# Performance work log

Measured on AMD Instinct MI355X. Metric: run time of the kernel, lower is better.

## Reference

```python
import jax, jax.numpy as jnp
import numpy as np

NUM_HEADS = 16
NEG = -10000000.0


def setup_inputs() -> dict:
    key = jax.random.key(0)
    k1, k2, k3 = jax.random.split(key, 3)
    B, N, C = 4, 2048, 1024
    inputs = jax.random.normal(k1, (B, N, C), dtype=jnp.float32)
    # learned params (xavier-ish scale)
    W_qkv = jax.random.normal(k2, (C, 3 * C), dtype=jnp.float32) * 0.02
    W_proj = jax.random.normal(k3, (C, C), dtype=jnp.float32) * 0.02
    b_proj = jnp.zeros((C,), dtype=jnp.float32)
    attn_mask = jnp.ones((N, N), dtype=jnp.int32)      # >0 means keep
    padding_mask = jnp.zeros((B, N), dtype=jnp.int32)  # >0 means mask out
    return {"inputs": inputs, "attn_mask": attn_mask, "padding_mask": padding_mask,
            "W_qkv": W_qkv, "W_proj": W_proj, "b_proj": b_proj}


def reference(inputs, attn_mask, padding_mask, W_qkv, W_proj, b_proj):
    B, N, C = inputs.shape
    H = NUM_HEADS
    d = C // H
    scale = d ** -0.5
    qkv = inputs @ W_qkv                                   # [B,N,3C]
    qkv = qkv.reshape(B, N, 3, H, d).transpose(2, 0, 3, 1, 4)  # [3,B,H,N,d]
    q, k, v = qkv[0], qkv[1], qkv[2]
    scores = jnp.einsum('bhqd,bhkd->bhqk', q, k) * scale   # [B,H,N,N]
    scores = jnp.where(attn_mask > 0, scores, NEG)
    pm = padding_mask[:, None, None, :]                    # [B,1,1,N]
    scores = jnp.where(pm > 0, NEG, scores)
    attn = jax.nn.softmax(scores, axis=-1)
    x = jnp.einsum('bhqk,bhkd->bhqd', attn, v)             # [B,H,N,d]
    x = x.swapaxes(1, 2).reshape(B, N, C)
    return x @ W_proj + b_proj
```

## Files before the change

kernel.cpp:

```cpp
#include <hip/hip_runtime.h>

#define NEG -10000000.0f
#define QSCALE 0.18033688011112042f

typedef __attribute__((ext_vector_type(8))) short bf16x8;
typedef __attribute__((ext_vector_type(4))) float f32x4;

static __device__ __forceinline__ short f2bf(float f) {
    unsigned int u = __float_as_uint(f);
    unsigned int r = (u + 0x7fffu + ((u >> 16) & 1u)) >> 16;
    return (short)r;
}

static __device__ __forceinline__ unsigned pack_bf16_2(float a, float b) {
    unsigned ua = __float_as_uint(a) + 0x8000u;
    unsigned ub = __float_as_uint(b) + 0x8000u;
    return __builtin_amdgcn_perm(ub, ua, 0x07060302u);
}

static __device__ __forceinline__ void async_cp16(const void* g, void* l) {
    __builtin_amdgcn_global_load_lds(
        (const __attribute__((address_space(1))) unsigned int*)g,
        (__attribute__((address_space(3))) unsigned int*)l, 16, 0, 0);
}

__global__ void cvt_bf16(const float* __restrict__ src, short* __restrict__ dst, int n4) {
    int i = blockIdx.x * blockDim.x + threadIdx.x;
    if (i < n4) {
        float4 v = reinterpret_cast<const float4*>(src)[i];
        short4 o;
        o.x = f2bf(v.x); o.y = f2bf(v.y); o.z = f2bf(v.z); o.w = f2bf(v.w);
        reinterpret_cast<short4*>(dst)[i] = o;
    }
}

__global__ void transpose_cvt(const float* __restrict__ src, short* __restrict__ dst,
                              int rows, int cols) {
    __shared__ float tile[32][33];
    int bx = blockIdx.x * 32;
    int by = blockIdx.y * 32;
    int tx = threadIdx.x & 31, ty = threadIdx.x >> 5;
    for (int j = 0; j < 4; ++j)
        tile[ty + j * 8][tx] = src[(size_t)(by + ty + j * 8) * cols + bx + tx];
    __syncthreads();
    for (int j = 0; j < 4; ++j)
        dst[(size_t)(bx + ty + j * 8) * rows + by + tx] = f2bf(tile[tx][ty + j * 8]);
}

__global__ void mask_flags(const int* __restrict__ attn_mask, int* __restrict__ flags) {
    int blk = blockIdx.x;
    int qt = blk >> 5, kt = blk & 31;
    int tid = threadIdx.x;
    __shared__ int blockok;
    if (tid == 0) blockok = 1;
    __syncthreads();
    int ok = 1;
    for (int j = 0; j < 32; ++j) {
        int idx = j * 256 + tid;
        int qr = qt * 128 + (idx >> 6);
        int kc = kt * 64 + (idx & 63);
        ok &= (attn_mask[(size_t)qr * 2048 + kc] != 0);
    }
    if (!ok) blockok = 0;
    __syncthreads();
    if (tid == 0) flags[blk] = blockok;
}

__global__ void pad_flags(const int* __restrict__ padding, int* __restrict__ pf) {
    int t = threadIdx.x;
    int b = t >> 5, kt = t & 31;
    int any = 0;
    for (int j = 0; j < 64; ++j) any |= (padding[b * 2048 + kt * 64 + j] > 0);
    pf[t] = any;
}

__global__ __launch_bounds__(256, 2) void gemm_bf16(
    const short* __restrict__ A, const short* __restrict__ Bt, int mode,
    short* __restrict__ q_ws, short* __restrict__ k_ws, short* __restrict__ v_ws,
    float* __restrict__ out, const float* __restrict__ bias) {
    const int K = 1024;
    __shared__ short As[128][64];
    __shared__ short Bs[128][64];
    int tid = threadIdx.x, lane = tid & 63, w = tid >> 6;
    int wm = w & 1, wn = w >> 1;
    int m0 = blockIdx.y * 128, n0 = blockIdx.x * 128;
    int col = lane & 15, quad = lane >> 4;
    int l8 = lane >> 3, j8 = lane & 7;

    f32x4 acc[4][4] = {};

    for (int k0 = 0; k0 < K; k0 += 64) {
        for (int c = 0; c < 4; ++c) {
            int rr = w * 32 + c * 8 + l8;
            int sw = (j8 ^ (rr & 7)) << 3;
            async_cp16(&A[(size_t)(m0 + rr) * K + k0 + sw], &As[w * 32 + c * 8][0]);
            async_cp16(&Bt[(size_t)(n0 + rr) * K + k0 + sw], &Bs[w * 32 + c * 8][0]);
        }
        __syncthreads();
        for (int ks = 0; ks < 2; ++ks) {
            bf16x8 af[4], bfr[4];
            for (int mt = 0; mt < 4; ++mt)
                af[mt] = *reinterpret_cast<const bf16x8*>(
                    &As[wm * 64 + mt * 16 + col][((ks * 4 + quad) ^ (col & 7)) << 3]);
            for (int nt = 0; nt < 4; ++nt)
                bfr[nt] = *reinterpret_cast<const bf16x8*>(
                    &Bs[wn * 64 + nt * 16 + col][((ks * 4 + quad) ^ (col & 7)) << 3]);
            for (int mt = 0; mt < 4; ++mt)
                for (int nt = 0; nt < 4; ++nt)
                    acc[mt][nt] = __builtin_amdgcn_mfma_f32_16x16x32_bf16(af[mt], bfr[nt], acc[mt][nt], 0, 0, 0);
        }
        __syncthreads();
    }

    if (mode == 0) {
        int which = n0 >> 10;
        int cb = n0 & 1023;
        if (which == 2) {
            for (int mt = 0; mt < 4; ++mt) {
                int m = m0 + wm * 64 + mt * 16 + quad * 4;
                int b = m >> 11, n = m & 2047;
                for (int nt = 0; nt < 4; ++nt) {
                    int c = cb + wn * 64 + nt * 16 + col;
                    int h = c >> 6, dd = c & 63;
                    short4 pk;
                    for (int r = 0; r < 4; ++r) ((short*)&pk)[r] = f2bf(acc[mt][nt][r]);
                    *reinterpret_cast<short4*>(&v_ws[((size_t)((b * 16 + h) * 64 + dd)) * 2048 + n]) = pk;
                }
            }
        } else {
            short* dst = (which == 0) ? q_ws : k_ws;
            float scl = (which == 0) ? QSCALE : 1.0f;
            for (int mt = 0; mt < 4; ++mt)
                for (int nt = 0; nt < 4; ++nt)
                    for (int r = 0; r < 4; ++r) {
                        int m = m0 + wm * 64 + mt * 16 + quad * 4 + r;
                        int c = cb + wn * 64 + nt * 16 + col;
                        int b = m >> 11, n = m & 2047;
                        int h = c >> 6, dd = c & 63;
                        dst[((size_t)(b * 16 + h) * 2048 + n) * 64 + dd] = f2bf(acc[mt][nt][r] * scl);
                    }
        }
    } else {
        for (int mt = 0; mt < 4; ++mt)
            for (int nt = 0; nt < 4; ++nt)
                for (int r = 0; r < 4; ++r) {
                    int m = m0 + wm * 64 + mt * 16 + quad * 4 + r;
                    int c = n0 + wn * 64 + nt * 16 + col;
                    out[(size_t)m * 1024 + c] = acc[mt][nt][r] + bias[c];
                }
    }
}

__global__ __launch_bounds__(256, 4) void flash_attn(
    const short* __restrict__ q_ws, const short* __restrict__ k_ws,
    const short* __restrict__ v_ws, const int* __restrict__ aflags,
    const int* __restrict__ pflags, const int* __restrict__ padding,
    const int* __restrict__ attn_mask, short* __restrict__ xb) {
    const int Nn = 2048, D = 64;
    __shared__ short QP[128][64];
    __shared__ short Ks[64][64];
    __shared__ short Vt[64][64];
    __shared__ __align__(16) float padb[64];

    int tid = threadIdx.x, lane = tid & 63, w = tid >> 6;
    int col = lane & 15, quad = lane >> 4;
    int bh = blockIdx.y, b = bh >> 4, h = bh & 15;
    int q0 = blockIdx.x * 128, qt = blockIdx.x;
    int l8 = lane >> 3, j8 = lane & 7;

    for (int c = 0; c < 4; ++c) {
        int rr = w * 32 + c * 8 + l8;
        async_cp16(&q_ws[((size_t)bh * Nn + q0 + rr) * D + ((j8 ^ (rr & 7)) << 3)],
                   &QP[w * 32 + c * 8][0]);
    }
    __syncthreads();

    bf16x8 qf[2][2];
    for (int t = 0; t < 2; ++t)
        for (int ks = 0; ks < 2; ++ks)
            qf[t][ks] = *reinterpret_cast<const bf16x8*>(
                &QP[w * 32 + t * 16 + col][((ks * 4 + quad) ^ (col & 7)) << 3]);

    f32x4 oacc[2][4] = {};
    f32x4 lacc[2] = {};

    for (int kt = 0; kt < 32; ++kt) {
        int k0 = kt * 64;
        for (int c = 0; c < 2; ++c) {
            int rr = w * 16 + c * 8 + l8;
            int sw = (j8 ^ (rr & 7)) << 3;
            async_cp16(&k_ws[((size_t)bh * Nn + k0 + rr) * D + sw], &Ks[w * 16 + c * 8][0]);
            async_cp16(&v_ws[((size_t)bh * D + rr) * Nn + k0 + sw], &Vt[w * 16 + c * 8][0]);
        }
        int pflag = pflags[b * 32 + kt];
        if (pflag && tid < 64) padb[tid] = (padding[b * Nn + k0 + tid] > 0) ? NEG : 0.f;
        __syncthreads();

        f32x4 sacc[4][2] = {};
        for (int ks = 0; ks < 2; ++ks) {
            bf16x8 kf[4];
            for (int mt = 0; mt < 4; ++mt)
                kf[mt] = *reinterpret_cast<const bf16x8*>(
                    &Ks[mt * 16 + col][((ks * 4 + quad) ^ (col & 7)) << 3]);
            for (int mt = 0; mt < 4; ++mt)
                for (int t = 0; t < 2; ++t)
                    sacc[mt][t] = __builtin_amdgcn_mfma_f32_16x16x32_bf16(kf[mt], qf[t][ks], sacc[mt][t], 0, 0, 0);
        }

        if (!aflags[qt * 32 + kt]) {
            for (int mt = 0; mt < 4; ++mt)
                for (int t = 0; t < 2; ++t)
                    for (int r = 0; r < 4; ++r) {
                        int kc = k0 + mt * 16 + quad * 4 + r;
                        int qr = q0 + w * 32 + t * 16 + col;
                        if (attn_mask[(size_t)qr * Nn + kc] == 0) sacc[mt][t][r] = NEG;
                    }
        }
        if (pflag) {
            for (int mt = 0; mt < 4; ++mt) {
                f32x4 pb = *reinterpret_cast<const f32x4*>(&padb[mt * 16 + quad * 4]);
                for (int t = 0; t < 2; ++t)
                    for (int r = 0; r < 4; ++r) sacc[mt][t][r] += pb[r];
            }
        }

        for (int t = 0; t < 2; ++t) {
            int qrow = w * 32 + t * 16 + col;
            for (int mt = 0; mt < 4; ++mt) {
                f32x4 e;
                e[0] = __builtin_amdgcn_exp2f(sacc[mt][t][0]);
                e[1] = __builtin_amdgcn_exp2f(sacc[mt][t][1]);
                e[2] = __builtin_amdgcn_exp2f(sacc[mt][t][2]);
                e[3] = __builtin_amdgcn_exp2f(sacc[mt][t][3]);
                lacc[t] += e;
                unsigned p0 = pack_bf16_2(e[0], e[1]);
                unsigned p1 = pack_bf16_2(e[2], e[3]);
                int chunk = (mt * 2 + (quad >> 1)) ^ (col & 7);
                *reinterpret_cast<uint2*>(&QP[qrow][(chunk << 3) + ((quad & 1) << 2)]) =
                    make_uint2(p0, p1);
            }
        }

        for (int ks = 0; ks < 2; ++ks) {
            bf16x8 pf[2], vf[4];
            for (int t = 0; t < 2; ++t)
                pf[t] = *reinterpret_cast<const bf16x8*>(
                    &QP[w * 32 + t * 16 + col][((ks * 4 + quad) ^ (col & 7)) << 3]);
            for (int nt = 0; nt < 4; ++nt)
                vf[nt] = *reinterpret_cast<const bf16x8*>(
                    &Vt[nt * 16 + col][((ks * 4 + quad) ^ (col & 7)) << 3]);
            for (int t = 0; t < 2; ++t)
                for (int nt = 0; nt < 4; ++nt)
                    oacc[t][nt] = __builtin_amdgcn_mfma_f32_16x16x32_bf16(pf[t], vf[nt], oacc[t][nt], 0, 0, 0);
        }
        __syncthreads();
    }

    for (int t = 0; t < 2; ++t) {
        float ls = lacc[t][0] + lacc[t][1] + lacc[t][2] + lacc[t][3];
        ls += __shfl_xor(ls, 16);
        ls += __shfl_xor(ls, 32);
        for (int r = 0; r < 4; ++r) {
            float lv = __shfl(ls, quad * 4 + r, 16);
            float inv = 1.f / lv;
            int n = q0 + w * 32 + t * 16 + quad * 4 + r;
            for (int nt = 0; nt < 4; ++nt) {
                int dd = nt * 16 + col;
                xb[((size_t)(b * Nn + n)) * 1024 + h * 64 + dd] = f2bf(oacc[t][nt][r] * inv);
            }
        }
    }
}

extern "C" void kernel_launch(void* const* d_in, const int* in_sizes, int n_in,
                              void* d_out, int out_size, void* d_ws, size_t ws_size,
                              hipStream_t stream) {
    const float* x        = (const float*)d_in[0];
    const int* attn_mask  = (const int*)d_in[1];
    const int* padding    = (const int*)d_in[2];
    const float* W_qkv    = (const float*)d_in[3];
    const float* W_proj   = (const float*)d_in[4];
    const float* b_proj   = (const float*)d_in[5];
    float* out            = (float*)d_out;

    char* ws = (char*)d_ws;
    short* Xb   = (short*)(ws);
    short* Wqt  = (short*)(ws + (16u << 20));
    short* Wpt  = (short*)(ws + (22u << 20));
    short* q_ws = (short*)(ws + (24u << 20));
    short* k_ws = (short*)(ws + (40u << 20));
    short* v_ws = (short*)(ws + (56u << 20));
    short* xbuf = (short*)(ws + (72u << 20));
    int*  flags = (int*)(ws + (88u << 20));

    cvt_bf16<<<8192, 256, 0, stream>>>(x, Xb, 8388608 / 4);
    transpose_cvt<<<dim3(3072 / 32, 1024 / 32), 256, 0, stream>>>(W_qkv, Wqt, 1024, 3072);
    transpose_cvt<<<dim3(1024 / 32, 1024 / 32), 256, 0, stream>>>(W_proj, Wpt, 1024, 1024);
    mask_flags<<<512, 256, 0, stream>>>(attn_mask, flags);
    pad_flags<<<1, 128, 0, stream>>>(padding, flags + 512);

    gemm_bf16<<<dim3(3072 / 128, 8192 / 128), 256, 0, stream>>>(
        Xb, Wqt, 0, q_ws, k_ws, v_ws, nullptr, nullptr);

    flash_attn<<<dim3(16, 64), 256, 0, stream>>>(
        q_ws, k_ws, v_ws, flags, flags + 512, padding, attn_mask, xbuf);

    gemm_bf16<<<dim3(1024 / 128, 8192 / 128), 256, 0, stream>>>(
        xbuf, Wpt, 1, nullptr, nullptr, nullptr, out, b_proj);
}
```

Before: 294.9 us.

## Double-buffer K tiles in LDS and load V fragments directly from global

The flash-attention kernel now double-buffers the K tile and padding bias in shared memory. The next tile's async copy is issued before the current tile's QK MFMAs, which removes the per-iteration barrier that waited on fresh loads. V is no longer staged through LDS: each lane reads its bf16x8 V fragments straight from global memory into registers, split into two halves so the second load overlaps the softmax work. This cuts LDS traffic and footprint, but it adds strided global reads of V per wave that depend on cache hits, and more live registers.

```diff
diff --git a/kernel.cpp b/kernel.cpp
--- a/kernel.cpp
+++ b/kernel.cpp
@@ -158,21 +158,28 @@
     const int* __restrict__ attn_mask, short* __restrict__ xb) {
     const int Nn = 2048, D = 64;
     __shared__ short QP[128][64];
-    __shared__ short Ks[64][64];
-    __shared__ short Vt[64][64];
-    __shared__ __align__(16) float padb[64];
+    __shared__ short Ks[2][64][64];
+    __shared__ __align__(16) float padb[2][64];
 
     int tid = threadIdx.x, lane = tid & 63, w = tid >> 6;
     int col = lane & 15, quad = lane >> 4;
     int bh = blockIdx.y, b = bh >> 4, h = bh & 15;
     int q0 = blockIdx.x * 128, qt = blockIdx.x;
     int l8 = lane >> 3, j8 = lane & 7;
-
-    for (int c = 0; c < 4; ++c) {
-        int rr = w * 32 + c * 8 + l8;
-        async_cp16(&q_ws[((size_t)bh * Nn + q0 + rr) * D + ((j8 ^ (rr & 7)) << 3)],
-                   &QP[w * 32 + c * 8][0]);
-    }
+    int swz = (j8 ^ l8) << 3;
+
+    {
+        const short* qg = q_ws + ((size_t)bh * Nn + q0 + w * 32 + l8) * D + swz;
+        async_cp16(qg,          &QP[w * 32][0]);
+        async_cp16(qg + 8 * D,  &QP[w * 32 + 8][0]);
+        async_cp16(qg + 16 * D, &QP[w * 32 + 16][0]);
+        async_cp16(qg + 24 * D, &QP[w * 32 + 24][0]);
+    }
+    const short* kg = k_ws + ((size_t)bh * Nn + w * 16 + l8) * D + swz;
+    async_cp16(kg,         &Ks[0][w * 16][0]);
+    async_cp16(kg + 8 * D, &Ks[0][w * 16 + 8][0]);
+    if (pflags[b * 32] && tid < 64)
+        padb[0][tid] = (padding[b * Nn + tid] > 0) ? NEG : 0.f;
     __syncthreads();
 
     bf16x8 qf[2][2];
@@ -185,27 +192,30 @@
     f32x4 lacc[2] = {};
 
     for (int kt = 0; kt < 32; ++kt) {
+        int cur = kt & 1;
         int k0 = kt * 64;
-        for (int c = 0; c < 2; ++c) {
-            int rr = w * 16 + c * 8 + l8;
-            int sw = (j8 ^ (rr & 7)) << 3;
-            async_cp16(&k_ws[((size_t)bh * Nn + k0 + rr) * D + sw], &Ks[w * 16 + c * 8][0]);
-            async_cp16(&v_ws[((size_t)bh * D + rr) * Nn + k0 + sw], &Vt[w * 16 + c * 8][0]);
-        }
-        int pflag = pflags[b * 32 + kt];
-        if (pflag && tid < 64) padb[tid] = (padding[b * Nn + k0 + tid] > 0) ? NEG : 0.f;
-        __syncthreads();
+
+        if (kt < 31) {
+            const short* kn = kg + (size_t)(kt + 1) * 64 * D;
+            async_cp16(kn,         &Ks[cur ^ 1][w * 16][0]);
+            async_cp16(kn + 8 * D, &Ks[cur ^ 1][w * 16 + 8][0]);
+            if (pflags[b * 32 + kt + 1] && tid < 64)
+                padb[cur ^ 1][tid] = (padding[b * Nn + k0 + 64 + tid] > 0) ? NEG : 0.f;
+        }
 
         f32x4 sacc[4][2] = {};
-        for (int ks = 0; ks < 2; ++ks) {
-            bf16x8 kf[4];
-            for (int mt = 0; mt < 4; ++mt)
-                kf[mt] = *reinterpret_cast<const bf16x8*>(
-                    &Ks[mt * 16 + col][((ks * 4 + quad) ^ (col & 7)) << 3]);
-            for (int mt = 0; mt < 4; ++mt)
-                for (int t = 0; t < 2; ++t)
-                    sacc[mt][t] = __builtin_amdgcn_mfma_f32_16x16x32_bf16(kf[mt], qf[t][ks], sacc[mt][t], 0, 0, 0);
-        }
+        for (int ks = 0; ks < 2; ++ks)
+            for (int mt = 0; mt < 4; ++mt) {
+                bf16x8 kf = *reinterpret_cast<const bf16x8*>(
+                    &Ks[cur][mt * 16 + col][((ks * 4 + quad) ^ (col & 7)) << 3]);
+                sacc[mt][0] = __builtin_amdgcn_mfma_f32_16x16x32_bf16(kf, qf[0][ks], sacc[mt][0], 0, 0, 0);
+                sacc[mt][1] = __builtin_amdgcn_mfma_f32_16x16x32_bf16(kf, qf[1][ks], sacc[mt][1], 0, 0, 0);
+            }
+
+        const short* vg = v_ws + ((size_t)bh * D + col) * Nn + k0 + quad * 8;
+        bf16x8 vf0[4], vf1[4];
+        for (int nt = 0; nt < 4; ++nt)
+            vf0[nt] = *reinterpret_cast<const bf16x8*>(vg + (size_t)nt * 16 * Nn);
 
         if (!aflags[qt * 32 + kt]) {
             for (int mt = 0; mt < 4; ++mt)
@@ -216,9 +226,9 @@
                         if (attn_mask[(size_t)qr * Nn + kc] == 0) sacc[mt][t][r] = NEG;
                     }
         }
-        if (pflag) {
+        if (pflags[b * 32 + kt]) {
             for (int mt = 0; mt < 4; ++mt) {
-                f32x4 pb = *reinterpret_cast<const f32x4*>(&padb[mt * 16 + quad * 4]);
+                f32x4 pb = *reinterpret_cast<const f32x4*>(&padb[cur][mt * 16 + quad * 4]);
                 for (int t = 0; t < 2; ++t)
                     for (int r = 0; r < 4; ++r) sacc[mt][t][r] += pb[r];
             }
@@ -241,18 +251,22 @@
             }
         }
 
-        for (int ks = 0; ks < 2; ++ks) {
-            bf16x8 pf[2], vf[4];
-            for (int t = 0; t < 2; ++t)
-                pf[t] = *reinterpret_cast<const bf16x8*>(
-                    &QP[w * 32 + t * 16 + col][((ks * 4 + quad) ^ (col & 7)) << 3]);
+        for (int nt = 0; nt < 4; ++nt)
+            vf1[nt] = *reinterpret_cast<const bf16x8*>(vg + (size_t)nt * 16 * Nn + 32);
+
+        for (int t = 0; t < 2; ++t) {
+            bf16x8 pf = *reinterpret_cast<const bf16x8*>(
+                &QP[w * 32 + t * 16 + col][(quad ^ (col & 7)) << 3]);
             for (int nt = 0; nt < 4; ++nt)
-                vf[nt] = *reinterpret_cast<const bf16x8*>(
-                    &Vt[nt * 16 + col][((ks * 4 + quad) ^ (col & 7)) << 3]);
-            for (int t = 0; t < 2; ++t)
-                for (int nt = 0; nt < 4; ++nt)
-                    oacc[t][nt] = __builtin_amdgcn_mfma_f32_16x16x32_bf16(pf[t], vf[nt], oacc[t][nt], 0, 0, 0);
-        }
+                oacc[t][nt] = __builtin_amdgcn_mfma_f32_16x16x32_bf16(pf, vf0[nt], oacc[t][nt], 0, 0, 0);
+        }
+        for (int t = 0; t < 2; ++t) {
+            bf16x8 pf = *reinterpret_cast<const bf16x8*>(
+                &QP[w * 32 + t * 16 + col][((4 + quad) ^ (col & 7)) << 3]);
+            for (int nt = 0; nt < 4; ++nt)
+                oacc[t][nt] = __builtin_amdgcn_mfma_f32_16x16x32_bf16(pf, vf1[nt], oacc[t][nt], 0, 0, 0);
+        }
+
         __syncthreads();
     }
 
```

After: 366.8 us. 24.4% more time.
